# Optimization experiments

Measured on AMD Instinct MI355X. Metric: run time of the kernel, lower is better.

## Reference

```python
import jax, jax.numpy as jnp
import numpy as np

HDIM = 1024
N_CLASSES = 50257
CUTOFFS = [2000, 10000, N_CLASSES]  # shortlist=2000, clusters: [2000,10000), [10000,50257)
DIV = 4.0
HEAD_SIZE = CUTOFFS[0] + 2  # shortlist + 2 cluster logits


def setup_inputs() -> dict:
    key = jax.random.key(0)
    ks = jax.random.split(key, 12)
    B, S, K = 8, 512, 256
    N = B * K
    hsz0 = int(HDIM // (DIV ** 1))  # 256
    hsz1 = int(HDIM // (DIV ** 2))  # 64
    osz0 = CUTOFFS[1] - CUTOFFS[0]  # 8000
    osz1 = CUTOFFS[2] - CUTOFFS[1]  # 40257
    w = 0.02
    return {
        "targets": jax.random.randint(ks[0], (N,), 0, N_CLASSES),
        "last_hidden_states": jax.random.normal(ks[1], (B, S, HDIM), dtype=jnp.float32),
        "cls_tokens_batch": jax.random.normal(ks[2], (B, HDIM), dtype=jnp.float32),
        "idx": jax.random.randint(ks[3], (B, K), 0, S),
        "head_W": jax.random.normal(ks[4], (HEAD_SIZE, HDIM), dtype=jnp.float32) * w,
        "head_b": jnp.zeros((HEAD_SIZE,), dtype=jnp.float32),
        "proj0_W": jax.random.normal(ks[5], (hsz0, HDIM), dtype=jnp.float32) * w,
        "out0_W": jax.random.normal(ks[6], (osz0, hsz0), dtype=jnp.float32) * w,
        "proj1_W": jax.random.normal(ks[7], (hsz1, HDIM), dtype=jnp.float32) * w,
        "out1_W": jax.random.normal(ks[8], (osz1, hsz1), dtype=jnp.float32) * w,
    }


def reference(targets, last_hidden_states, cls_tokens_batch, idx,
              head_W, head_b, proj0_W, out0_W, proj1_W, out1_W):
    # Gather context token embeddings: [B, K, H] -> [N, H]
    B, S, H = last_hidden_states.shape
    x = last_hidden_states[jnp.arange(B)[:, None], idx].reshape(-1, H)
    N = x.shape[0]
    c0, c1 = CUTOFFS[0], CUTOFFS[1]

    # Head: shortlist logits + per-cluster routing logits, [N, c0+2]
    head_logprob = jax.nn.log_softmax(x @ head_W.T + head_b, axis=-1)
    # Tail clusters: low-rank projection then output GEMM + log-softmax
    lp0 = jax.nn.log_softmax((x @ proj0_W.T) @ out0_W.T, axis=-1)  # [N, 8000]
    lp1 = jax.nn.log_softmax((x @ proj1_W.T) @ out1_W.T, axis=-1)  # [N, 40257]

    n = jnp.arange(N)
    t = targets
    short = head_logprob[n, jnp.clip(t, 0, c0 - 1)]
    mid = head_logprob[:, c0] + lp0[n, jnp.clip(t - c0, 0, lp0.shape[1] - 1)]
    high = head_logprob[:, c0 + 1] + lp1[n, jnp.clip(t - c1, 0, lp1.shape[1] - 1)]
    out = jnp.where(t < c0, short, jnp.where(t < c1, mid, high))  # target log-probs [N]
    loss = -jnp.mean(out)
    return out, loss
```

## Files before the change

### kernel.cpp

```cpp
#include <hip/hip_runtime.h>
#include <hip/hip_bf16.h>

#define NROWS 2048
#define L2E 1.4426950408889634f

typedef float f32x4 __attribute__((ext_vector_type(4)));
typedef __bf16 bf16x8 __attribute__((ext_vector_type(8)));
typedef short s16x8 __attribute__((ext_vector_type(8)));

typedef const __attribute__((address_space(1))) unsigned int* gas_t;
typedef __attribute__((address_space(3))) unsigned int* las_t;

__device__ __forceinline__ unsigned short f2bf(float f) {
    unsigned int u = __float_as_uint(f);
    unsigned int r = (u + 0x7FFFu + ((u >> 16) & 1u)) >> 16;
    return (unsigned short)r;
}
__device__ __forceinline__ float bf2f(unsigned short u) {
    return __uint_as_float((unsigned int)u << 16);
}
__device__ __forceinline__ f32x4 mfma16(s16x8 a, s16x8 b, f32x4 c) {
    return __builtin_amdgcn_mfma_f32_16x16x32_bf16(
        __builtin_bit_cast(bf16x8, a), __builtin_bit_cast(bf16x8, b), c, 0, 0, 0);
}

__global__ void k_prologue(const float* __restrict__ lhs, const int* __restrict__ idx,
                           const float* __restrict__ hw, const float* __restrict__ p0w,
                           const float* __restrict__ p1w, const float* __restrict__ o0w,
                           const float* __restrict__ o1w, const float* __restrict__ hb,
                           const int* __restrict__ tgt,
                           unsigned short* __restrict__ xb, unsigned short* __restrict__ hWb,
                           unsigned short* __restrict__ pW01, unsigned short* __restrict__ o0Wb,
                           unsigned short* __restrict__ o1Wb,
                           float* __restrict__ bias_s, int* __restrict__ tc,
                           unsigned long long* __restrict__ lossacc,
                           unsigned int* __restrict__ ticket) {
    int bid = blockIdx.x;
    if (bid < 2048) {
        int tid = bid * 256 + threadIdx.x;
        int n = tid >> 8;
        int c = (tid & 255) << 2;
        int b = n >> 8, k = n & 255;
        int srow = idx[(b << 8) + k];
        const float4 v = *reinterpret_cast<const float4*>(
            lhs + (((size_t)b << 9) + srow) * 1024 + c);
        ushort4 o = make_ushort4(f2bf(v.x), f2bf(v.y), f2bf(v.z), f2bf(v.w));
        *reinterpret_cast<ushort4*>(xb + (size_t)n * 1024 + c) = o;
        return;
    }
    bid -= 2048;
    if (bid < 6968) {
        const long B0 = 2048L * 1024;
        const long B1 = B0 + 384L * 1024;
        const long B2 = B1 + 8064L * 256;
        const long B3 = B2 + 40320L * 64;
        long e = ((long)bid * 256 + threadIdx.x) * 4;
        if (e >= B3) return;
        const float* src; unsigned short* dst; long rows; int colshift; long base;
        float sc;
        if (e < B0)      { base = 0;  src = hw;  dst = hWb;  rows = 2002;  colshift = 10; sc = L2E; }
        else if (e < B1) {
            long l = e - B0;
            long row = l >> 10;
            unsigned short* d = pW01 + l;
            ushort4 o;
            if (row < 256) {
                float4 v = *reinterpret_cast<const float4*>(p0w + l);
                o = make_ushort4(f2bf(v.x), f2bf(v.y), f2bf(v.z), f2bf(v.w));
            } else if (row < 320) {
                float4 v = *reinterpret_cast<const float4*>(p1w + (l - 256L * 1024));
                o = make_ushort4(f2bf(v.x), f2bf(v.y), f2bf(v.z), f2bf(v.w));
            } else {
                o = make_ushort4(0, 0, 0, 0);
            }
            *reinterpret_cast<ushort4*>(d) = o;
            return;
        }
        else if (e < B2) { base = B1; src = o0w; dst = o0Wb; rows = 8000;  colshift = 8; sc = L2E; }
        else             { base = B2; src = o1w; dst = o1Wb; rows = 40257; colshift = 6; sc = L2E; }
        long l = e - base;
        long row = l >> colshift;
        ushort4 o;
        if (row < rows) {
            float4 v = *reinterpret_cast<const float4*>(src + l);
            o = make_ushort4(f2bf(v.x * sc), f2bf(v.y * sc), f2bf(v.z * sc), f2bf(v.w * sc));
        } else {
            o = make_ushort4(0, 0, 0, 0);
        }
        *reinterpret_cast<ushort4*>(dst + l) = o;
        return;
    }
    bid -= 6968;
    int n = bid * 256 + threadIdx.x;
    if (n >= 2048) return;
    if (n == 0) { *lossacc = 0ull; *ticket = 0u; }
    bias_s[n] = (n < 2002) ? hb[n] * L2E : -1e30f;
    int t = tgt[n];
    tc[n] = min(t, 1999);
    tc[2048 + n] = min(max(t - 2000, 0), 7999);
    tc[4096 + n] = min(max(t - 10000, 0), 40256);
}

template <int NT>
__global__ __launch_bounds__(256)
void k_mm(const unsigned short* __restrict__ A, int lda,
          const unsigned short* __restrict__ B, int ldb,
          const float* __restrict__ bias, float* __restrict__ partial,
          unsigned short* __restrict__ hout, int hstride, int hcols, int fsplit) {
    __shared__ unsigned short As[2][64 * 64];
    __shared__ unsigned short Bs[2][128 * 64];
    const int tid = threadIdx.x;
    const int lane = tid & 63, wid = tid >> 6;
    const int wc = wid;
    const int g = lane >> 4, cl = lane & 15;
    const int row0 = blockIdx.x * 64;
    const int col0 = blockIdx.y * 128;

    const int sr = wid * 8 + (lane >> 3);
    const int swz = ((lane & 7) ^ (lane >> 3)) * 8;
    const unsigned short* Ab = A + (size_t)(row0 + sr) * lda + swz;
    const unsigned short* Bb = B + (size_t)(col0 + sr) * ldb + swz;

    auto stage = [&](int buf, int kt) {
        unsigned short* la = &As[buf][wid * 8 * 64];
        unsigned short* lb = &Bs[buf][wid * 8 * 64];
#pragma unroll
        for (int i = 0; i < 2; ++i)
            __builtin_amdgcn_global_load_lds((gas_t)(const void*)(Ab + kt + (size_t)i * 32 * lda),
                                             (las_t)(void*)(la + i * 32 * 64), 16, 0, 0);
#pragma unroll
        for (int i = 0; i < 4; ++i)
            __builtin_amdgcn_global_load_lds((gas_t)(const void*)(Bb + kt + (size_t)i * 32 * ldb),
                                             (las_t)(void*)(lb + i * 32 * 64), 16, 0, 0);
    };

    f32x4 acc[4][2] = {};
    stage(0, 0);
    asm volatile("s_waitcnt vmcnt(0)" ::: "memory");
    __builtin_amdgcn_s_barrier();
    const int sA = (cl & 7);
    for (int t = 0; t < NT; ++t) {
        if (t + 1 < NT) stage((t + 1) & 1, (t + 1) * 64);
        const unsigned short* Al = &As[t & 1][cl * 64];
        const unsigned short* Bl = &Bs[t & 1][(wc * 32 + cl) * 64];
#pragma unroll
        for (int kk2 = 0; kk2 < 2; ++kk2) {
            const int slot = ((kk2 * 4 + g) ^ sA) * 8;
            s16x8 a[4], b[2];
#pragma unroll
            for (int mi = 0; mi < 4; ++mi)
                a[mi] = *reinterpret_cast<const s16x8*>(Al + mi * 16 * 64 + slot);
#pragma unroll
            for (int ni = 0; ni < 2; ++ni)
                b[ni] = *reinterpret_cast<const s16x8*>(Bl + ni * 16 * 64 + slot);
#pragma unroll
            for (int mi = 0; mi < 4; ++mi)
#pragma unroll
                for (int ni = 0; ni < 2; ++ni)
                    acc[mi][ni] = mfma16(a[mi], b[ni], acc[mi][ni]);
        }
        if (t + 1 < NT) {
            asm volatile("s_waitcnt vmcnt(0)" ::: "memory");
            __builtin_amdgcn_s_barrier();
        }
    }

    if ((int)blockIdx.y >= fsplit) {
        int c0 = col0 - fsplit * 128;
#pragma unroll
        for (int mi = 0; mi < 4; ++mi)
#pragma unroll
            for (int ni = 0; ni < 2; ++ni) {
                int col = c0 + wc * 32 + ni * 16 + cl;
                if (col < hcols) {
#pragma unroll
                    for (int r = 0; r < 4; ++r) {
                        int row = row0 + mi * 16 + g * 4 + r;
                        hout[(size_t)row * hstride + col] = f2bf(acc[mi][ni][r]);
                    }
                }
            }
    } else {
        float bv0 = bias[col0 + wc * 32 + cl];
        float bv1 = bias[col0 + wc * 32 + 16 + cl];
        int strip = blockIdx.y * 4 + wc;
#pragma unroll
        for (int mi = 0; mi < 4; ++mi)
#pragma unroll
            for (int r = 0; r < 4; ++r) {
                float s = __builtin_amdgcn_exp2f(acc[mi][0][r] + bv0)
                        + __builtin_amdgcn_exp2f(acc[mi][1][r] + bv1);
                s += __shfl_xor(s, 1, 64);
                s += __shfl_xor(s, 2, 64);
                s += __shfl_xor(s, 4, 64);
                s += __shfl_xor(s, 8, 64);
                if (cl == 0)
                    partial[(size_t)strip * NROWS + row0 + mi * 16 + g * 4 + r] = s;
            }
    }
}

#define OUT1_IT 5
__global__ __launch_bounds__(256)
void k_tail(const unsigned short* __restrict__ h01, const unsigned short* __restrict__ o0Wb,
            const unsigned short* __restrict__ o1Wb, const unsigned short* __restrict__ xb,
            const float* __restrict__ headW, const float* __restrict__ hb,
            const float* __restrict__ o0w, const float* __restrict__ o1w,
            const int* __restrict__ tc,
            float* __restrict__ p0, float* __restrict__ p1,
            float* __restrict__ tgh, float* __restrict__ r0, float* __restrict__ r1,
            float* __restrict__ tg0, float* __restrict__ tg1) {
    __shared__ unsigned short smem[4][128 * 64];
    const int tid = threadIdx.x;
    const int lane = tid & 63, wid = tid >> 6;
    const int wr = wid >> 1, wc = wid & 1;
    const int g = lane >> 4, cl = lane & 15;
    int bid = blockIdx.x;

    if (bid < 1008) {
        const int row0 = (bid & 15) * 128;
        const int col0 = (bid >> 4) * 128;
        const int sr = wid * 8 + (lane >> 3);
        const int swz = ((lane & 7) ^ (lane >> 3)) * 8;
        const unsigned short* Ab = h01 + (size_t)(row0 + sr) * 320 + swz;
        const unsigned short* Bb = o0Wb + (size_t)(col0 + sr) * 256 + swz;
        auto stage = [&](int buf, int kt) {
            unsigned short* la = &smem[buf][wid * 8 * 64];
            unsigned short* lb = &smem[2 + buf][wid * 8 * 64];
#pragma unroll
            for (int i = 0; i < 4; ++i) {
                __builtin_amdgcn_global_load_lds((gas_t)(const void*)(Ab + kt + (size_t)i * 32 * 320),
                                                 (las_t)(void*)(la + i * 32 * 64), 16, 0, 0);
                __builtin_amdgcn_global_load_lds((gas_t)(const void*)(Bb + kt + (size_t)i * 32 * 256),
                                                 (las_t)(void*)(lb + i * 32 * 64), 16, 0, 0);
            }
        };
        f32x4 acc[4][4] = {};
        stage(0, 0);
        asm volatile("s_waitcnt vmcnt(0)" ::: "memory");
        __builtin_amdgcn_s_barrier();
        const int sA = (cl & 7);
        for (int t = 0; t < 4; ++t) {
            if (t < 3) stage((t + 1) & 1, (t + 1) * 64);
            const unsigned short* Al = &smem[t & 1][(wr * 64 + cl) * 64];
            const unsigned short* Bl = &smem[2 + (t & 1)][(wc * 64 + cl) * 64];
#pragma unroll
            for (int kk2 = 0; kk2 < 2; ++kk2) {
                const int slot = ((kk2 * 4 + g) ^ sA) * 8;
                s16x8 a[4], b[4];
#pragma unroll
                for (int mi = 0; mi < 4; ++mi)
                    a[mi] = *reinterpret_cast<const s16x8*>(Al + mi * 16 * 64 + slot);
#pragma unroll
                for (int ni = 0; ni < 4; ++ni)
                    b[ni] = *reinterpret_cast<const s16x8*>(Bl + ni * 16 * 64 + slot);
#pragma unroll
                for (int mi = 0; mi < 4; ++mi)
#pragma unroll
                    for (int ni = 0; ni < 4; ++ni)
                        acc[mi][ni] = mfma16(a[mi], b[ni], acc[mi][ni]);
            }
            if (t < 3) {
                asm volatile("s_waitcnt vmcnt(0)" ::: "memory");
                __builtin_amdgcn_s_barrier();
            }
        }
        int strip = (bid >> 4) * 2 + wc;
#pragma unroll
        for (int mi = 0; mi < 4; ++mi)
#pragma unroll
            for (int r = 0; r < 4; ++r) {
                float s = 0.f;
#pragma unroll
                for (int ni = 0; ni < 4; ++ni)
                    s += __builtin_amdgcn_exp2f(acc[mi][ni][r]);
                s += __shfl_xor(s, 1, 64);
                s += __shfl_xor(s, 2, 64);
                s += __shfl_xor(s, 4, 64);
                s += __shfl_xor(s, 8, 64);
                if (cl == 0)
                    p0[(size_t)strip * NROWS + row0 + wr * 64 + mi * 16 + g * 4 + r] = s;
            }
        return;
    }
    if (bid < 2016) {
        bid -= 1008;
        const int row0 = (bid & 15) * 128 + wr * 64;
        const int yb = bid >> 4;
        const int t0 = yb * OUT1_IT;
        s16x8 a[4][2];
#pragma unroll
        for (int mi = 0; mi < 4; ++mi)
#pragma unroll
            for (int kk = 0; kk < 2; ++kk)
                a[mi][kk] = *reinterpret_cast<const s16x8*>(
                    h01 + (size_t)(row0 + mi * 16 + cl) * 320 + 256 + kk * 32 + g * 8);
        const int sr = wid * 8 + (lane >> 3);
        const int swz = ((lane & 7) ^ (lane >> 3)) * 8;
        auto stage = [&](int buf, int tile) {
            const unsigned short* gb = o1Wb + ((size_t)tile * 128 + sr) * 64 + swz;
            unsigned short* lb = &smem[buf][wid * 8 * 64];
#pragma unroll
            for (int i = 0; i < 4; ++i)
                __builtin_amdgcn_global_load_lds((gas_t)(const void*)(gb + (size_t)i * 32 * 64),
                                                 (las_t)(void*)(lb + i * 32 * 64), 16, 0, 0);
        };
        float sexp[4][4] = {};
        const f32x4 z4 = {0.f, 0.f, 0.f, 0.f};
        stage(0, t0);
        asm volatile("s_waitcnt vmcnt(0)" ::: "memory");
        __builtin_amdgcn_s_barrier();
        int buf = 0;
        const int sA = (cl & 7);
#pragma unroll 1
        for (int it = 0; it < OUT1_IT; ++it) {
            if (it + 1 < OUT1_IT) stage(buf ^ 1, t0 + it + 1);
            const unsigned short* Bl = smem[buf];
#pragma unroll
            for (int ni = 0; ni < 4; ++ni) {
                const unsigned short* br = Bl + (wc * 64 + ni * 16 + cl) * 64;
                s16x8 b0 = *reinterpret_cast<const s16x8*>(br + (g ^ sA) * 8);
                s16x8 b1 = *reinterpret_cast<const s16x8*>(br + ((4 + g) ^ sA) * 8);
                f32x4 acc[4];
#pragma unroll
                for (int mi = 0; mi < 4; ++mi)
                    acc[mi] = mfma16(a[mi][0], b0, z4);
#pragma unroll
                for (int mi = 0; mi < 4; ++mi)
                    acc[mi] = mfma16(a[mi][1], b1, acc[mi]);
#pragma unroll
                for (int mi = 0; mi < 4; ++mi)
#pragma unroll
                    for (int r = 0; r < 4; ++r)
                        sexp[mi][r] += __builtin_amdgcn_exp2f(acc[mi][r]);
            }
            if (it + 1 < OUT1_IT) {
                asm volatile("s_waitcnt vmcnt(0)" ::: "memory");
                __builtin_amdgcn_s_barrier();
                buf ^= 1;
            }
        }
#pragma unroll
        for (int mi = 0; mi < 4; ++mi)
#pragma unroll
            for (int r = 0; r < 4; ++r) {
                float s = sexp[mi][r];
                s += __shfl_xor(s, 1, 64);
                s += __shfl_xor(s, 2, 64);
                s += __shfl_xor(s, 4, 64);
                s += __shfl_xor(s, 8, 64);
                if (cl == 0)
                    p1[(size_t)(yb * 2 + wc) * NROWS + row0 + mi * 16 + g * 4 + r] = s;
            }
        return;
    }
    bid -= 2016;
    int n = (bid * 256 + tid) >> 6;
    int tch = tc[n], tc0 = tc[2048 + n], tc1 = tc[4096 + n];
    const unsigned short* xr = xb + (size_t)n * 1024 + lane * 16;
    s16x8 x0 = *reinterpret_cast<const s16x8*>(xr);
    s16x8 x1 = *reinterpret_cast<const s16x8*>(xr + 8);
    const float* wh = headW + (size_t)tch * 1024 + lane * 16;
    const float* wa = headW + (size_t)2000 * 1024 + lane * 16;
    const float* wb = headW + (size_t)2001 * 1024 + lane * 16;
    float dh = 0.f, da = 0.f, db = 0.f;
#pragma unroll
    for (int i = 0; i < 8; ++i) {
        float xv = bf2f((unsigned short)x0[i]);
        dh += xv * wh[i]; da += xv * wa[i]; db += xv * wb[i];
    }
#pragma unroll
    for (int i = 0; i < 8; ++i) {
        float xv = bf2f((unsigned short)x1[i]);
        dh += xv * wh[8 + i]; da += xv * wa[8 + i]; db += xv * wb[8 + i];
    }
    ushort4 h0v = *reinterpret_cast<const ushort4*>(h01 + (size_t)n * 320 + lane * 4);
    float4 w0v = *reinterpret_cast<const float4*>(o0w + (size_t)tc0 * 256 + lane * 4);
    float d2 = bf2f(h0v.x) * w0v.x + bf2f(h0v.y) * w0v.y +
               bf2f(h0v.z) * w0v.z + bf2f(h0v.w) * w0v.w;
    float d3 = bf2f(h01[(size_t)n * 320 + 256 + lane]) * o1w[(size_t)tc1 * 64 + lane];
#pragma unroll
    for (int m = 1; m < 64; m <<= 1) {
        dh += __shfl_xor(dh, m, 64);
        da += __shfl_xor(da, m, 64);
        db += __shfl_xor(db, m, 64);
        d2 += __shfl_xor(d2, m, 64);
        d3 += __shfl_xor(d3, m, 64);
    }
    if (lane == 0) {
        tgh[n] = dh + hb[tch];
        r0[n] = da + hb[2000];
        r1[n] = db + hb[2001];
        tg0[n] = d2;
        tg1[n] = d3;
    }
}

__global__ void k_finalize(const float* __restrict__ ph, const float* __restrict__ p0,
                           const float* __restrict__ p1, const float* __restrict__ tgh,
                           const float* __restrict__ r0, const float* __restrict__ r1,
                           const float* __restrict__ tg0, const float* __restrict__ tg1,
                           const int* __restrict__ tgt, float* __restrict__ outv,
                           unsigned long long* __restrict__ lossacc,
                           unsigned int* __restrict__ ticket) {
    int n = blockIdx.x * 128 + threadIdx.x;
    float sh = 0.f, s0 = 0.f, s1 = 0.f;
    for (int s = 0; s < 64; ++s) sh += ph[(size_t)s * NROWS + n];
    for (int s = 0; s < 126; ++s) s0 += p0[(size_t)s * NROWS + n];
    for (int s = 0; s < 126; ++s) s1 += p1[(size_t)s * NROWS + n];
    s0 -= 64.f;
    s1 -= 63.f;
    float lh = __logf(sh), l0 = __logf(s0), l1 = __logf(s1);
    int t = tgt[n];
    float o;
    if (t < 2000) o = tgh[n] - lh;
    else if (t < 10000) o = (r0[n] - lh) + (tg0[n] - l0);
    else o = (r1[n] - lh) + (tg1[n] - l1);
    outv[n] = o;
    __shared__ float red[128];
    red[threadIdx.x] = o;
    __syncthreads();
    for (int s = 64; s > 0; s >>= 1) {
        if (threadIdx.x < s) red[threadIdx.x] += red[threadIdx.x + s];
        __syncthreads();
    }
    if (threadIdx.x == 0) {
        long long fx = __double2ll_rn((double)red[0] * 1048576.0);
        atomicAdd(lossacc, (unsigned long long)fx);
        __threadfence();
        unsigned int tk = atomicAdd(ticket, 1u);
        if (tk == 15u) {
            unsigned long long v = atomicAdd(lossacc, 0ull);
            long long sv = (long long)v;
            outv[NROWS] = (float)(-((double)sv / 1048576.0) / 2048.0);
        }
    }
}

extern "C" void kernel_launch(void* const* d_in, const int* in_sizes, int n_in,
                              void* d_out, int out_size, void* d_ws, size_t ws_size,
                              hipStream_t stream) {
    const int* targets   = (const int*)d_in[0];
    const float* lhs     = (const float*)d_in[1];
    const int* idx       = (const int*)d_in[3];
    const float* head_W  = (const float*)d_in[4];
    const float* head_b  = (const float*)d_in[5];
    const float* proj0_W = (const float*)d_in[6];
    const float* out0_W  = (const float*)d_in[7];
    const float* proj1_W = (const float*)d_in[8];
    const float* out1_W  = (const float*)d_in[9];

    char* ws = (char*)d_ws;
    size_t off = 0;
    auto alloc = [&](size_t bytes) -> void* {
        void* p = ws + off;
        off += (bytes + 255) & ~(size_t)255;
        return p;
    };

    unsigned short* xb   = (unsigned short*)alloc((size_t)2048 * 1024 * 2);
    unsigned short* wB   = (unsigned short*)alloc((size_t)2432 * 1024 * 2);
    unsigned short* hWb  = wB;
    unsigned short* pW01 = wB + (size_t)2048 * 1024;
    unsigned short* o0Wb = (unsigned short*)alloc((size_t)8064 * 256 * 2);
    unsigned short* o1Wb = (unsigned short*)alloc((size_t)40320 * 64 * 2);
    unsigned short* h01  = (unsigned short*)alloc((size_t)2048 * 320 * 2);
    float* ph  = (float*)alloc((size_t)64 * 2048 * 4);
    float* p0  = (float*)alloc((size_t)126 * 2048 * 4);
    float* p1  = (float*)alloc((size_t)126 * 2048 * 4);
    float* tgh = (float*)alloc(2048 * 4);
    float* r0  = (float*)alloc(2048 * 4);
    float* r1  = (float*)alloc(2048 * 4);
    float* tg0 = (float*)alloc(2048 * 4);
    float* tg1 = (float*)alloc(2048 * 4);
    int*   tc  = (int*)alloc(3 * 2048 * 4);
    float* bias_s = (float*)alloc(2048 * 4);
    unsigned long long* lossacc = (unsigned long long*)alloc(8);
    unsigned int* ticket = (unsigned int*)alloc(4);

    k_prologue<<<9024, 256, 0, stream>>>(lhs, idx, head_W, proj0_W, proj1_W, out0_W, out1_W,
                                         head_b, targets,
                                         xb, hWb, pW01, o0Wb, o1Wb, bias_s, tc,
                                         lossacc, ticket);

    k_mm<16><<<dim3(32, 19), 256, 0, stream>>>(
        xb, 1024, wB, 1024, bias_s, ph, h01, 320, 320, 16);

    k_tail<<<2528, 256, 0, stream>>>(h01, o0Wb, o1Wb, xb, head_W, head_b, out0_W, out1_W,
                                     tc, p0, p1, tgh, r0, r1, tg0, tg1);

    float* outv = (float*)d_out;
    k_finalize<<<16, 128, 0, stream>>>(ph, p0, p1, tgh, r0, r1, tg0, tg1, targets,
                                       outv, lossacc, ticket);
}
```

Baseline: 87.51 us.

## Fuse finalize into tail kernel via ticket and retile out0 GEMM to 64x128

Removes the separate finalize launch. The last 16 blocks of the tail kernel to take a ticket spin until every tail block is done, then reduce the partial sums and compute the outputs and the loss. The out0 GEMM tiles shrink from 128x128 to 64x128, doubling its block count and the number of partial-sum strips. The tail blocks are reordered so the out1 work is scheduled first, and launch bounds request 3 blocks per CU. The spin-wait needs all blocks to make forward progress and adds atomic traffic, and the final reduction now reads more partials.

Result: slower. 228.1 us (+160.6%).

```diff
diff --git a/kernel.cpp b/kernel.cpp
--- a/kernel.cpp
+++ b/kernel.cpp
@@ -3,6 +3,7 @@
 
 #define NROWS 2048
 #define L2E 1.4426950408889634f
+#define TAIL_BLOCKS 3536u
 
 typedef float f32x4 __attribute__((ext_vector_type(4)));
 typedef __bf16 bf16x8 __attribute__((ext_vector_type(8)));
@@ -34,7 +35,8 @@
                            unsigned short* __restrict__ o1Wb,
                            float* __restrict__ bias_s, int* __restrict__ tc,
                            unsigned long long* __restrict__ lossacc,
-                           unsigned int* __restrict__ ticket) {
+                           unsigned int* __restrict__ ticket,
+                           unsigned int* __restrict__ ticket2) {
     int bid = blockIdx.x;
     if (bid < 2048) {
         int tid = bid * 256 + threadIdx.x;
@@ -93,7 +95,7 @@
     bid -= 6968;
     int n = bid * 256 + threadIdx.x;
     if (n >= 2048) return;
-    if (n == 0) { *lossacc = 0ull; *ticket = 0u; }
+    if (n == 0) { *lossacc = 0ull; *ticket = 0u; *ticket2 = 0u; }
     bias_s[n] = (n < 2002) ? hb[n] * L2E : -1e30f;
     int t = tgt[n];
     tc[n] = min(t, 1999);
@@ -201,90 +203,29 @@
 }
 
 #define OUT1_IT 5
-__global__ __launch_bounds__(256)
+__global__ __launch_bounds__(256, 3)
 void k_tail(const unsigned short* __restrict__ h01, const unsigned short* __restrict__ o0Wb,
             const unsigned short* __restrict__ o1Wb, const unsigned short* __restrict__ xb,
             const float* __restrict__ headW, const float* __restrict__ hb,
             const float* __restrict__ o0w, const float* __restrict__ o1w,
-            const int* __restrict__ tc,
+            const int* __restrict__ tc, const int* __restrict__ tgt,
+            const float* __restrict__ ph,
             float* __restrict__ p0, float* __restrict__ p1,
             float* __restrict__ tgh, float* __restrict__ r0, float* __restrict__ r1,
-            float* __restrict__ tg0, float* __restrict__ tg1) {
-    __shared__ unsigned short smem[4][128 * 64];
+            float* __restrict__ tg0, float* __restrict__ tg1,
+            float* __restrict__ outv,
+            unsigned long long* __restrict__ lossacc,
+            unsigned int* __restrict__ ticket, unsigned int* __restrict__ ticket2) {
+    __shared__ unsigned short smemB[2][128 * 64];
+    __shared__ unsigned short smemA[2][64 * 64];
+    __shared__ unsigned int tkS;
     const int tid = threadIdx.x;
     const int lane = tid & 63, wid = tid >> 6;
-    const int wr = wid >> 1, wc = wid & 1;
     const int g = lane >> 4, cl = lane & 15;
     int bid = blockIdx.x;
 
     if (bid < 1008) {
-        const int row0 = (bid & 15) * 128;
-        const int col0 = (bid >> 4) * 128;
-        const int sr = wid * 8 + (lane >> 3);
-        const int swz = ((lane & 7) ^ (lane >> 3)) * 8;
-        const unsigned short* Ab = h01 + (size_t)(row0 + sr) * 320 + swz;
-        const unsigned short* Bb = o0Wb + (size_t)(col0 + sr) * 256 + swz;
-        auto stage = [&](int buf, int kt) {
-            unsigned short* la = &smem[buf][wid * 8 * 64];
-            unsigned short* lb = &smem[2 + buf][wid * 8 * 64];
-#pragma unroll
-            for (int i = 0; i < 4; ++i) {
-                __builtin_amdgcn_global_load_lds((gas_t)(const void*)(Ab + kt + (size_t)i * 32 * 320),
-                                                 (las_t)(void*)(la + i * 32 * 64), 16, 0, 0);
-                __builtin_amdgcn_global_load_lds((gas_t)(const void*)(Bb + kt + (size_t)i * 32 * 256),
-                                                 (las_t)(void*)(lb + i * 32 * 64), 16, 0, 0);
-            }
-        };
-        f32x4 acc[4][4] = {};
-        stage(0, 0);
-        asm volatile("s_waitcnt vmcnt(0)" ::: "memory");
-        __builtin_amdgcn_s_barrier();
-        const int sA = (cl & 7);
-        for (int t = 0; t < 4; ++t) {
-            if (t < 3) stage((t + 1) & 1, (t + 1) * 64);
-            const unsigned short* Al = &smem[t & 1][(wr * 64 + cl) * 64];
-            const unsigned short* Bl = &smem[2 + (t & 1)][(wc * 64 + cl) * 64];
-#pragma unroll
-            for (int kk2 = 0; kk2 < 2; ++kk2) {
-                const int slot = ((kk2 * 4 + g) ^ sA) * 8;
-                s16x8 a[4], b[4];
-#pragma unroll
-                for (int mi = 0; mi < 4; ++mi)
-                    a[mi] = *reinterpret_cast<const s16x8*>(Al + mi * 16 * 64 + slot);
-#pragma unroll
-                for (int ni = 0; ni < 4; ++ni)
-                    b[ni] = *reinterpret_cast<const s16x8*>(Bl + ni * 16 * 64 + slot);
-#pragma unroll
-                for (int mi = 0; mi < 4; ++mi)
-#pragma unroll
-                    for (int ni = 0; ni < 4; ++ni)
-                        acc[mi][ni] = mfma16(a[mi], b[ni], acc[mi][ni]);
-            }
-            if (t < 3) {
-                asm volatile("s_waitcnt vmcnt(0)" ::: "memory");
-                __builtin_amdgcn_s_barrier();
-            }
-        }
-        int strip = (bid >> 4) * 2 + wc;
-#pragma unroll
-        for (int mi = 0; mi < 4; ++mi)
-#pragma unroll
-            for (int r = 0; r < 4; ++r) {
-                float s = 0.f;
-#pragma unroll
-                for (int ni = 0; ni < 4; ++ni)
-                    s += __builtin_amdgcn_exp2f(acc[mi][ni][r]);
-                s += __shfl_xor(s, 1, 64);
-                s += __shfl_xor(s, 2, 64);
-                s += __shfl_xor(s, 4, 64);
-                s += __shfl_xor(s, 8, 64);
-                if (cl == 0)
-                    p0[(size_t)strip * NROWS + row0 + wr * 64 + mi * 16 + g * 4 + r] = s;
-            }
-        return;
-    }
-    if (bid < 2016) {
-        bid -= 1008;
+        const int wr = wid >> 1, wc = wid & 1;
         const int row0 = (bid & 15) * 128 + wr * 64;
         const int yb = bid >> 4;
         const int t0 = yb * OUT1_IT;
@@ -299,7 +240,7 @@
         const int swz = ((lane & 7) ^ (lane >> 3)) * 8;
         auto stage = [&](int buf, int tile) {
             const unsigned short* gb = o1Wb + ((size_t)tile * 128 + sr) * 64 + swz;
-            unsigned short* lb = &smem[buf][wid * 8 * 64];
+            unsigned short* lb = &smemB[buf][wid * 8 * 64];
 #pragma unroll
             for (int i = 0; i < 4; ++i)
                 __builtin_amdgcn_global_load_lds((gas_t)(const void*)(gb + (size_t)i * 32 * 64),
@@ -315,7 +256,7 @@
 #pragma unroll 1
         for (int it = 0; it < OUT1_IT; ++it) {
             if (it + 1 < OUT1_IT) stage(buf ^ 1, t0 + it + 1);
-            const unsigned short* Bl = smem[buf];
+            const unsigned short* Bl = smemB[buf];
 #pragma unroll
             for (int ni = 0; ni < 4; ++ni) {
                 const unsigned short* br = Bl + (wc * 64 + ni * 16 + cl) * 64;
@@ -352,87 +293,161 @@
                 if (cl == 0)
                     p1[(size_t)(yb * 2 + wc) * NROWS + row0 + mi * 16 + g * 4 + r] = s;
             }
-        return;
-    }
-    bid -= 2016;
-    int n = (bid * 256 + tid) >> 6;
-    int tch = tc[n], tc0 = tc[2048 + n], tc1 = tc[4096 + n];
-    const unsigned short* xr = xb + (size_t)n * 1024 + lane * 16;
-    s16x8 x0 = *reinterpret_cast<const s16x8*>(xr);
-    s16x8 x1 = *reinterpret_cast<const s16x8*>(xr + 8);
-    const float* wh = headW + (size_t)tch * 1024 + lane * 16;
-    const float* wa = headW + (size_t)2000 * 1024 + lane * 16;
-    const float* wb = headW + (size_t)2001 * 1024 + lane * 16;
-    float dh = 0.f, da = 0.f, db = 0.f;
-#pragma unroll
-    for (int i = 0; i < 8; ++i) {
-        float xv = bf2f((unsigned short)x0[i]);
-        dh += xv * wh[i]; da += xv * wa[i]; db += xv * wb[i];
-    }
-#pragma unroll
-    for (int i = 0; i < 8; ++i) {
-        float xv = bf2f((unsigned short)x1[i]);
-        dh += xv * wh[8 + i]; da += xv * wa[8 + i]; db += xv * wb[8 + i];
-    }
-    ushort4 h0v = *reinterpret_cast<const ushort4*>(h01 + (size_t)n * 320 + lane * 4);
-    float4 w0v = *reinterpret_cast<const float4*>(o0w + (size_t)tc0 * 256 + lane * 4);
-    float d2 = bf2f(h0v.x) * w0v.x + bf2f(h0v.y) * w0v.y +
-               bf2f(h0v.z) * w0v.z + bf2f(h0v.w) * w0v.w;
-    float d3 = bf2f(h01[(size_t)n * 320 + 256 + lane]) * o1w[(size_t)tc1 * 64 + lane];
-#pragma unroll
-    for (int m = 1; m < 64; m <<= 1) {
-        dh += __shfl_xor(dh, m, 64);
-        da += __shfl_xor(da, m, 64);
-        db += __shfl_xor(db, m, 64);
-        d2 += __shfl_xor(d2, m, 64);
-        d3 += __shfl_xor(d3, m, 64);
-    }
-    if (lane == 0) {
-        tgh[n] = dh + hb[tch];
-        r0[n] = da + hb[2000];
-        r1[n] = db + hb[2001];
-        tg0[n] = d2;
-        tg1[n] = d3;
-    }
-}
-
-__global__ void k_finalize(const float* __restrict__ ph, const float* __restrict__ p0,
-                           const float* __restrict__ p1, const float* __restrict__ tgh,
-                           const float* __restrict__ r0, const float* __restrict__ r1,
-                           const float* __restrict__ tg0, const float* __restrict__ tg1,
-                           const int* __restrict__ tgt, float* __restrict__ outv,
-                           unsigned long long* __restrict__ lossacc,
-                           unsigned int* __restrict__ ticket) {
-    int n = blockIdx.x * 128 + threadIdx.x;
+    } else if (bid < 3024) {
+        int b = bid - 1008;
+        const int row0 = (b & 31) * 64;
+        const int col0 = (b >> 5) * 128;
+        const int sr = wid * 8 + (lane >> 3);
+        const int swz = ((lane & 7) ^ (lane >> 3)) * 8;
+        const unsigned short* Ab = h01 + (size_t)(row0 + sr) * 320 + swz;
+        const unsigned short* Bb = o0Wb + (size_t)(col0 + sr) * 256 + swz;
+        auto stage = [&](int buf, int kt) {
+            unsigned short* la = &smemA[buf][wid * 8 * 64];
+            unsigned short* lb = &smemB[buf][wid * 8 * 64];
+#pragma unroll
+            for (int i = 0; i < 2; ++i)
+                __builtin_amdgcn_global_load_lds((gas_t)(const void*)(Ab + kt + (size_t)i * 32 * 320),
+                                                 (las_t)(void*)(la + i * 32 * 64), 16, 0, 0);
+#pragma unroll
+            for (int i = 0; i < 4; ++i)
+                __builtin_amdgcn_global_load_lds((gas_t)(const void*)(Bb + kt + (size_t)i * 32 * 256),
+                                                 (las_t)(void*)(lb + i * 32 * 64), 16, 0, 0);
+        };
+        f32x4 acc[4][2] = {};
+        stage(0, 0);
+        asm volatile("s_waitcnt vmcnt(0)" ::: "memory");
+        __builtin_amdgcn_s_barrier();
+        const int sA = (cl & 7);
+        for (int t = 0; t < 4; ++t) {
+            if (t < 3) stage((t + 1) & 1, (t + 1) * 64);
+            const unsigned short* Al = &smemA[t & 1][cl * 64];
+            const unsigned short* Bl = &smemB[t & 1][(wid * 32 + cl) * 64];
+#pragma unroll
+            for (int kk2 = 0; kk2 < 2; ++kk2) {
+                const int slot = ((kk2 * 4 + g) ^ sA) * 8;
+                s16x8 a[4], bb[2];
+#pragma unroll
+                for (int mi = 0; mi < 4; ++mi)
+                    a[mi] = *reinterpret_cast<const s16x8*>(Al + mi * 16 * 64 + slot);
+#pragma unroll
+                for (int ni = 0; ni < 2; ++ni)
+                    bb[ni] = *reinterpret_cast<const s16x8*>(Bl + ni * 16 * 64 + slot);
+#pragma unroll
+                for (int mi = 0; mi < 4; ++mi)
+#pragma unroll
+                    for (int ni = 0; ni < 2; ++ni)
+                        acc[mi][ni] = mfma16(a[mi], bb[ni], acc[mi][ni]);
+            }
+            if (t < 3) {
+                asm volatile("s_waitcnt vmcnt(0)" ::: "memory");
+                __builtin_amdgcn_s_barrier();
+            }
+        }
+        int strip = (b >> 5) * 4 + wid;
+#pragma unroll
+        for (int mi = 0; mi < 4; ++mi)
+#pragma unroll
+            for (int r = 0; r < 4; ++r) {
+                float s = __builtin_amdgcn_exp2f(acc[mi][0][r])
+                        + __builtin_amdgcn_exp2f(acc[mi][1][r]);
+                s += __shfl_xor(s, 1, 64);
+                s += __shfl_xor(s, 2, 64);
+                s += __shfl_xor(s, 4, 64);
+                s += __shfl_xor(s, 8, 64);
+                if (cl == 0)
+                    p0[(size_t)strip * NROWS + row0 + mi * 16 + g * 4 + r] = s;
+            }
+    } else {
+        int b = bid - 3024;
+        int n = (b * 256 + tid) >> 6;
+        int tch = tc[n], tc0 = tc[2048 + n], tc1 = tc[4096 + n];
+        const unsigned short* xr = xb + (size_t)n * 1024 + lane * 16;
+        s16x8 x0 = *reinterpret_cast<const s16x8*>(xr);
+        s16x8 x1 = *reinterpret_cast<const s16x8*>(xr + 8);
+        const float* wh = headW + (size_t)tch * 1024 + lane * 16;
+        const float* wa = headW + (size_t)2000 * 1024 + lane * 16;
+        const float* wb = headW + (size_t)2001 * 1024 + lane * 16;
+        float dh = 0.f, da = 0.f, db = 0.f;
+#pragma unroll
+        for (int i = 0; i < 8; ++i) {
+            float xv = bf2f((unsigned short)x0[i]);
+            dh += xv * wh[i]; da += xv * wa[i]; db += xv * wb[i];
+        }
+#pragma unroll
+        for (int i = 0; i < 8; ++i) {
+            float xv = bf2f((unsigned short)x1[i]);
+            dh += xv * wh[8 + i]; da += xv * wa[8 + i]; db += xv * wb[8 + i];
+        }
+        ushort4 h0v = *reinterpret_cast<const ushort4*>(h01 + (size_t)n * 320 + lane * 4);
+        float4 w0v = *reinterpret_cast<const float4*>(o0w + (size_t)tc0 * 256 + lane * 4);
+        float d2 = bf2f(h0v.x) * w0v.x + bf2f(h0v.y) * w0v.y +
+                   bf2f(h0v.z) * w0v.z + bf2f(h0v.w) * w0v.w;
+        float d3 = bf2f(h01[(size_t)n * 320 + 256 + lane]) * o1w[(size_t)tc1 * 64 + lane];
+#pragma unroll
+        for (int m = 1; m < 64; m <<= 1) {
+            dh += __shfl_xor(dh, m, 64);
+            da += __shfl_xor(da, m, 64);
+            db += __shfl_xor(db, m, 64);
+            d2 += __shfl_xor(d2, m, 64);
+            d3 += __shfl_xor(d3, m, 64);
+        }
+        if (lane == 0) {
+            tgh[n] = dh + hb[tch];
+            r0[n] = da + hb[2000];
+            r1[n] = db + hb[2001];
+            tg0[n] = d2;
+            tg1[n] = d3;
+        }
+    }
+
+    __syncthreads();
+    if (tid == 0) {
+        __threadfence();
+        tkS = atomicAdd(ticket, 1u);
+    }
+    __syncthreads();
+    unsigned int tk = tkS;
+    if (tk < TAIL_BLOCKS - 16u) return;
+
+    if (tid == 0) {
+        while (atomicAdd(ticket, 0u) < TAIL_BLOCKS) __builtin_amdgcn_s_sleep(2);
+        __threadfence();
+    }
+    __syncthreads();
+
+    const int chunk = (int)(tk - (TAIL_BLOCKS - 16u));
+    const int half = tid & 1;
+    const int n = chunk * 128 + (tid >> 1);
     float sh = 0.f, s0 = 0.f, s1 = 0.f;
-    for (int s = 0; s < 64; ++s) sh += ph[(size_t)s * NROWS + n];
-    for (int s = 0; s < 126; ++s) s0 += p0[(size_t)s * NROWS + n];
-    for (int s = 0; s < 126; ++s) s1 += p1[(size_t)s * NROWS + n];
+    for (int s = half; s < 64; s += 2)  sh += ph[(size_t)s * NROWS + n];
+    for (int s = half; s < 252; s += 2) s0 += p0[(size_t)s * NROWS + n];
+    for (int s = half; s < 126; s += 2) s1 += p1[(size_t)s * NROWS + n];
+    sh += __shfl_xor(sh, 1, 64);
+    s0 += __shfl_xor(s0, 1, 64);
+    s1 += __shfl_xor(s1, 1, 64);
     s0 -= 64.f;
     s1 -= 63.f;
-    float lh = __logf(sh), l0 = __logf(s0), l1 = __logf(s1);
+    float lh = __logf(sh);
     int t = tgt[n];
     float o;
     if (t < 2000) o = tgh[n] - lh;
-    else if (t < 10000) o = (r0[n] - lh) + (tg0[n] - l0);
-    else o = (r1[n] - lh) + (tg1[n] - l1);
-    outv[n] = o;
-    __shared__ float red[128];
-    red[threadIdx.x] = o;
+    else if (t < 10000) o = (r0[n] - lh) + (tg0[n] - __logf(s0));
+    else o = (r1[n] - lh) + (tg1[n] - __logf(s1));
+    float* red = (float*)smemA;
+    if (half == 0) { outv[n] = o; red[tid >> 1] = o; }
     __syncthreads();
-    for (int s = 64; s > 0; s >>= 1) {
-        if (threadIdx.x < s) red[threadIdx.x] += red[threadIdx.x + s];
+    for (int s2 = 64; s2 > 0; s2 >>= 1) {
+        if (tid < s2) red[tid] += red[tid + s2];
         __syncthreads();
     }
-    if (threadIdx.x == 0) {
+    if (tid == 0) {
         long long fx = __double2ll_rn((double)red[0] * 1048576.0);
         atomicAdd(lossacc, (unsigned long long)fx);
         __threadfence();
-        unsigned int tk = atomicAdd(ticket, 1u);
-        if (tk == 15u) {
+        unsigned int t2 = atomicAdd(ticket2, 1u);
+        if (t2 == 15u) {
             unsigned long long v = atomicAdd(lossacc, 0ull);
-            long long sv = (long long)v;
-            outv[NROWS] = (float)(-((double)sv / 1048576.0) / 2048.0);
+            outv[NROWS] = (float)(-((double)(long long)v / 1048576.0) / 2048.0);
         }
     }
 }
@@ -466,7 +481,7 @@
     unsigned short* o1Wb = (unsigned short*)alloc((size_t)40320 * 64 * 2);
     unsigned short* h01  = (unsigned short*)alloc((size_t)2048 * 320 * 2);
     float* ph  = (float*)alloc((size_t)64 * 2048 * 4);
-    float* p0  = (float*)alloc((size_t)126 * 2048 * 4);
+    float* p0  = (float*)alloc((size_t)252 * 2048 * 4);
     float* p1  = (float*)alloc((size_t)126 * 2048 * 4);
     float* tgh = (float*)alloc(2048 * 4);
     float* r0  = (float*)alloc(2048 * 4);
@@ -476,20 +491,20 @@
     int*   tc  = (int*)alloc(3 * 2048 * 4);
     float* bias_s = (float*)alloc(2048 * 4);
     unsigned long long* lossacc = (unsigned long long*)alloc(8);
-    unsigned int* ticket = (unsigned int*)alloc(4);
+    unsigned int* ticket  = (unsigned int*)alloc(4);
+    unsigned int* ticket2 = (unsigned int*)alloc(4);
 
     k_prologue<<<9024, 256, 0, stream>>>(lhs, idx, head_W, proj0_W, proj1_W, out0_W, out1_W,
                                          head_b, targets,
                                          xb, hWb, pW01, o0Wb, o1Wb, bias_s, tc,
-                                         lossacc, ticket);
+                                         lossacc, ticket, ticket2);
 
     k_mm<16><<<dim3(32, 19), 256, 0, stream>>>(
         xb, 1024, wB, 1024, bias_s, ph, h01, 320, 320, 16);
 
-    k_tail<<<2528, 256, 0, stream>>>(h01, o0Wb, o1Wb, xb, head_W, head_b, out0_W, out1_W,
-                                     tc, p0, p1, tgh, r0, r1, tg0, tg1);
-
     float* outv = (float*)d_out;
-    k_finalize<<<16, 128, 0, stream>>>(ph, p0, p1, tgh, r0, r1, tg0, tg1, targets,
-                                       outv, lossacc, ticket);
-}
+    k_tail<<<TAIL_BLOCKS, 256, 0, stream>>>(h01, o0Wb, o1Wb, xb, head_W, head_b,
+                                            out0_W, out1_W, tc, targets, ph,
+                                            p0, p1, tgh, r0, r1, tg0, tg1,
+                                            outv, lossacc, ticket, ticket2);
+}
```
